# Kernel optimization log

Measured on AMD Instinct MI355X. Metric: run time of the kernel, lower is better.

The kernel has to match this reference:

```python
import jax, jax.numpy as jnp
import numpy as np

WSZ = 8          # window size (h == w)
DIM_HEAD = 32
EPS = 1e-5


def _rotate_half(t):
    t1, t2 = jnp.split(t, 2, axis=-1)
    return jnp.concatenate([-t2, t1], axis=-1)


def _window_rope(wsz_h, wsz_w, dim_head, base=10000.0):
    quarter = dim_head // 4
    freq = 1.0 / base ** (jnp.arange(quarter, dtype=jnp.float32) / quarter)
    th = jnp.arange(wsz_h, dtype=jnp.float32)[:, None] * freq[None, :]   # (wh, q)
    tw = jnp.arange(wsz_w, dtype=jnp.float32)[:, None] * freq[None, :]   # (ww, q)
    th = jnp.broadcast_to(th[:, None, :], (wsz_h, wsz_w, quarter)).reshape(wsz_h * wsz_w, quarter)
    tw = jnp.broadcast_to(tw[None, :, :], (wsz_h, wsz_w, quarter)).reshape(wsz_h * wsz_w, quarter)
    theta = jnp.concatenate([th, tw], axis=-1)                            # (L, d/2)
    cos = jnp.concatenate([jnp.cos(theta), jnp.cos(theta)], axis=-1)      # (L, d)
    sin = jnp.concatenate([jnp.sin(theta), jnp.sin(theta)], axis=-1)
    return cos, sin


def setup_inputs() -> dict:
    key = jax.random.key(0)
    k1, k2, k3 = jax.random.split(key, 3)
    B, D, H, W = 4, 512, 128, 128
    inner = 512  # heads * dim_head
    return {
        "x": jax.random.normal(k1, (B, D, H, W), dtype=jnp.float32),
        "ln_g": jnp.ones((D,), jnp.float32),
        "ln_b": jnp.zeros((D,), jnp.float32),
        "w_qkv": jax.random.normal(k2, (3 * inner, D), jnp.float32) * 0.02,
        "w_out": jax.random.normal(k3, (D, inner), jnp.float32) * 0.02,
        "b_out": jnp.zeros((D,), jnp.float32),
    }


def reference(x, ln_g, ln_b, w_qkv, w_out, b_out):
    B, D, H, W = x.shape
    wsz = WSZ
    dh = DIM_HEAD
    heads = D // dh
    nh, nw = H // wsz, W // wsz
    L = wsz * wsz
    shift = wsz // 2

    # channel LayerNorm (biased var over dim=1)
    mean = jnp.mean(x, axis=1, keepdims=True)
    var = jnp.var(x, axis=1, keepdims=True)
    xn = (x - mean) / jnp.sqrt(var + EPS) * ln_g[None, :, None, None] + ln_b[None, :, None, None]

    # shifted windows
    xs = jnp.roll(xn, shift=(-shift, -shift), axis=(-2, -1))
    # b d (h s1) (w s2) -> (b h w) d s1 s2
    xw = xs.reshape(B, D, nh, wsz, nw, wsz).transpose(0, 2, 4, 1, 3, 5)
    xw = xw.reshape(B * nh * nw, D, wsz, wsz)

    # 1x1 conv qkv (no bias)
    qkv = jnp.einsum('bdxy,ed->bexy', xw, w_qkv)           # (Bw, 3*inner, ws, ws)
    q, k, v = jnp.split(qkv, 3, axis=1)

    def to_heads(t):
        Bw = t.shape[0]
        return t.reshape(Bw, heads, dh, L).transpose(0, 1, 3, 2)  # (Bw, h, L, d)
    q, k, v = map(to_heads, (q, k, v))

    cos, sin = _window_rope(wsz, wsz, dh)
    cos = cos[None, None].astype(q.dtype)
    sin = sin[None, None].astype(q.dtype)
    q = q * cos + _rotate_half(q) * sin
    k = k * cos + _rotate_half(k) * sin

    scale = dh ** -0.5
    logits = jnp.einsum('bhid,bhjd->bhij', q, k) * scale
    attn = jax.nn.softmax(logits, axis=-1)
    out = jnp.einsum('bhij,bhjd->bhid', attn, v)            # (Bw, h, L, d)

    # b h (x y) d -> b (h d) x y
    out = out.transpose(0, 1, 3, 2).reshape(B * nh * nw, heads * dh, wsz, wsz)
    out = jnp.einsum('bdxy,ed->bexy', out, w_out) + b_out[None, :, None, None]

    # (b h w) d s1 s2 -> b d (h s1) (w s2)
    out = out.reshape(B, nh, nw, D, wsz, wsz).transpose(0, 3, 1, 4, 2, 5)
    out = out.reshape(B, D, H, W)
    out = jnp.roll(out, shift=(shift, shift), axis=(-2, -1))
    return out
```

## Files before the change

kernel.cpp:

```cpp
#include <hip/hip_runtime.h>
#include <hip/hip_bf16.h>

typedef unsigned short u16;
typedef __attribute__((ext_vector_type(8))) __bf16 bf16x8;
typedef __attribute__((ext_vector_type(4))) float f32x4;
typedef __attribute__((ext_vector_type(8))) unsigned short u16x8;

#define DEV __device__ __forceinline__

DEV float bf2f(u16 v){ union{unsigned u; float f;} c; c.u=((unsigned)v)<<16; return c.f; }
DEV u16 f2bf(float f){ union{float f; unsigned u;} c; c.f=f; unsigned r=c.u+0x7FFFu+((c.u>>16)&1u); return (u16)(r>>16); }
DEV f32x4 mfma16(bf16x8 a, bf16x8 b, f32x4 c){ return __builtin_amdgcn_mfma_f32_16x16x32_bf16(a,b,c,0,0,0); }


__global__ __launch_bounds__(256) void cvt_params_k(const float* __restrict__ wqkv, const float* __restrict__ wout,
                                                    const float* __restrict__ bout,
                                                    u16* __restrict__ wqkv_c, u16* __restrict__ wout_c,
                                                    u16* __restrict__ bout_c){
  int i = blockIdx.x*256 + threadIdx.x;
  if (i < 786432) wqkv_c[i] = f2bf(wqkv[i]);
  int j = i - 786432;
  if (j >= 0 && j < 262144) wout_c[j] = f2bf(wout[j]);
  int k = i - 1048576;
  if (k >= 0 && k < 512) bout_c[k] = f2bf(bout[k]);
}

__global__ __launch_bounds__(512) void ln_fused_k(const float* __restrict__ x, const float* __restrict__ g,
                                                  const float* __restrict__ bta, u16* __restrict__ A){
  __shared__ __align__(16) u16 tile[128*130];
  __shared__ float2 sstat[128];
  __shared__ float sg[512], sb2[512];
  float* reds = (float*)tile;
  float* redq = reds + 16*128;

  const int blk = blockIdx.x;
  const int b = blk >> 7, h_src = blk & 127;
  const int tid = threadIdx.x;
  const int wq = tid & 31, dr = tid >> 5;

  sg[tid]  = g[tid];
  sb2[tid] = bta[tid];

  const float* xp = x + ((size_t)(b*512)*128 + h_src)*128 + wq*4;

  float s0=0.f,s1=0.f,s2=0.f,s3=0.f, q0=0.f,q1=0.f,q2=0.f,q3=0.f;
  #pragma unroll 8
  for (int k = 0; k < 32; ++k){
    float4 v = *(const float4*)(xp + (size_t)(k*16 + dr)*16384);
    s0 += v.x; q0 += v.x*v.x;
    s1 += v.y; q1 += v.y*v.y;
    s2 += v.z; q2 += v.z*v.z;
    s3 += v.w; q3 += v.w*v.w;
  }
  *(float4*)&reds[dr*128 + wq*4] = make_float4(s0,s1,s2,s3);
  *(float4*)&redq[dr*128 + wq*4] = make_float4(q0,q1,q2,q3);
  __syncthreads();

  if (tid < 128){
    float s = 0.f, q = 0.f;
    #pragma unroll
    for (int r = 0; r < 16; ++r){ s += reds[r*128 + tid]; q += redq[r*128 + tid]; }
    float mean = s*(1.f/512.f);
    float rstd = rsqrtf(q*(1.f/512.f) - mean*mean + 1e-5f);
    sstat[tid] = make_float2(mean, rstd);
  }
  __syncthreads();

  const float2 st0 = sstat[wq*4+0];
  const float2 st1 = sstat[wq*4+1];
  const float2 st2 = sstat[wq*4+2];
  const float2 st3 = sstat[wq*4+3];

  const int h_out = (h_src - 4) & 127;
  const int mbase = ((b*16 + (h_out>>3))*16)*64 + (h_out&7)*8;
  const int seg = tid & 15, i0 = tid >> 4;

  for (int c = 0; c < 4; ++c){
    __syncthreads();
    #pragma unroll
    for (int k = 0; k < 8; ++k){
      const int d = c*128 + k*16 + dr;
      float4 v = *(const float4*)(xp + (size_t)d*16384);
      const float gg = sg[d], bb = sb2[d];
      u16* tr = tile + (size_t)(k*16 + dr)*130 + wq*4;
      tr[0] = f2bf((v.x - st0.x)*st0.y*gg + bb);
      tr[1] = f2bf((v.y - st1.x)*st1.y*gg + bb);
      tr[2] = f2bf((v.z - st2.x)*st2.y*gg + bb);
      tr[3] = f2bf((v.w - st3.x)*st3.y*gg + bb);
    }
    __syncthreads();
    #pragma unroll
    for (int p = 0; p < 4; ++p){
      const int i = p*32 + i0;
      const int w_out = (i - 4) & 127;
      const int m = mbase + (w_out>>3)*64 + (w_out&7);
      u16x8 o;
      #pragma unroll
      for (int jj = 0; jj < 8; ++jj) o[jj] = tile[(size_t)(seg*8 + jj)*130 + i];
      *(u16x8*)(A + (size_t)m*512 + c*128 + seg*8) = o;
    }
  }
}

template<bool BIAS>
__global__ __launch_bounds__(256) void gemm_nt_k(const u16* __restrict__ A, const u16* __restrict__ B,
                                                 const u16* __restrict__ bias, u16* __restrict__ C,
                                                 int M, int N, int K){
  __shared__ u16 As[128*32];
  __shared__ u16 Bs[128*32];
  const int tid = threadIdx.x, lane = tid & 63, wv = tid >> 6;
  const int q4 = lane >> 4, cc = lane & 15;
  const int m0 = blockIdx.y*128, n0 = blockIdx.x*128;
  const int wm = (wv >> 1)*64, wn = (wv & 1)*64;

  const int lrow = tid >> 2, lgrp = tid & 3;
  const u16* ag0 = A + (size_t)(m0 + lrow)*K + lgrp*8;
  const u16* ag1 = ag0 + (size_t)64*K;
  const u16* bg0 = B + (size_t)(n0 + lrow)*K + lgrp*8;
  const u16* bg1 = bg0 + (size_t)64*K;
  u16* as0 = As + tid*8;  u16* as1 = As + 2048 + tid*8;
  u16* bs0 = Bs + tid*8;  u16* bs1 = Bs + 2048 + tid*8;

  f32x4 acc[4][4] = {};
  for (int k0 = 0; k0 < K; k0 += 32){
    __builtin_amdgcn_global_load_lds(ag0 + k0, as0, 16, 0, 0);
    __builtin_amdgcn_global_load_lds(ag1 + k0, as1, 16, 0, 0);
    __builtin_amdgcn_global_load_lds(bg0 + k0, bs0, 16, 0, 0);
    __builtin_amdgcn_global_load_lds(bg1 + k0, bs1, 16, 0, 0);
    __syncthreads();
    bf16x8 af[4], bfr[4];
    #pragma unroll
    for (int t=0; t<4; ++t){
      u16x8 ta = *(const u16x8*)(As + (wm + t*16 + cc)*32 + q4*8);
      af[t]  = __builtin_bit_cast(bf16x8, ta);
      u16x8 tb = *(const u16x8*)(Bs + (wn + t*16 + cc)*32 + q4*8);
      bfr[t] = __builtin_bit_cast(bf16x8, tb);
    }
    #pragma unroll
    for (int i=0; i<4; ++i)
      #pragma unroll
      for (int j=0; j<4; ++j)
        acc[i][j] = mfma16(af[i], bfr[j], acc[i][j]);
    __syncthreads();
  }
  #pragma unroll
  for (int j=0; j<4; ++j){
    int col = n0 + wn + j*16 + cc;
    float bv = 0.f;
    if (BIAS) bv = bf2f(bias[col]);
    #pragma unroll
    for (int i=0; i<4; ++i){
      int rbase = m0 + wm + i*16 + q4*4;
      #pragma unroll
      for (int r=0; r<4; ++r)
        C[(size_t)(rbase + r)*N + col] = f2bf(acc[i][j][r] + bv);
    }
  }
}

__global__ __launch_bounds__(256) void attn_k(const u16* __restrict__ qkv, u16* __restrict__ O){
  __shared__ u16 Psh[4][64*72];
  const int tid = threadIdx.x, lane = tid & 63, wv = tid >> 6;
  const int q4 = lane >> 4, cc = lane & 15;
  const int w0 = blockIdx.x >> 2;
  const int hh = blockIdx.x & 3;
  const size_t base = (size_t)w0*64*1536;
  u16* Pw = Psh[wv];

  float freqj[8];
  #pragma unroll
  for (int j=0; j<8; ++j) freqj[j] = exp2f(-1.6609640474436811f * (float)j);
  const float sgn = (q4 < 2) ? -1.f : 1.f;
  const bool use_s2 = (q4 & 1) != 0;

  const int h = wv*4 + hh;
  bf16x8 qf[4], kf[4];
  #pragma unroll
  for (int t=0; t<4; ++t){
    const int l = t*16 + cc;
    const float sel = use_s2 ? (float)(l & 7) : (float)(l >> 3);
    u16x8 qr = *(const u16x8*)(qkv + base + (size_t)l*1536 + h*32 + q4*8);
    u16x8 kr = *(const u16x8*)(qkv + base + (size_t)l*1536 + 512 + h*32 + q4*8);
    u16x8 qo, ko;
    #pragma unroll
    for (int j=0; j<8; ++j){
      float qv = bf2f(qr[j]), kv = bf2f(kr[j]);
      float qp = __shfl_xor(qv, 32);
      float kp = __shfl_xor(kv, 32);
      float sn, cs; __sincosf(sel * freqj[j], &sn, &cs);
      qo[j] = f2bf(qv*cs + sgn*qp*sn);
      ko[j] = f2bf(kv*cs + sgn*kp*sn);
    }
    qf[t] = __builtin_bit_cast(bf16x8, qo);
    kf[t] = __builtin_bit_cast(bf16x8, ko);
  }
  f32x4 zero = {0.f, 0.f, 0.f, 0.f};
  f32x4 sacc[4][4];
  #pragma unroll
  for (int i=0; i<4; ++i)
    #pragma unroll
    for (int j=0; j<4; ++j)
      sacc[i][j] = mfma16(qf[i], kf[j], zero);
  const float scale = 0.17677669529663689f;
  #pragma unroll
  for (int i=0; i<4; ++i){
    #pragma unroll
    for (int r=0; r<4; ++r){
      float v0 = sacc[i][0][r]*scale, v1 = sacc[i][1][r]*scale;
      float v2 = sacc[i][2][r]*scale, v3 = sacc[i][3][r]*scale;
      float mx = fmaxf(fmaxf(v0,v1), fmaxf(v2,v3));
      #pragma unroll
      for (int msk=1; msk<16; msk<<=1) mx = fmaxf(mx, __shfl_xor(mx, msk));
      float e0 = __expf(v0-mx), e1 = __expf(v1-mx), e2 = __expf(v2-mx), e3 = __expf(v3-mx);
      float sm = e0+e1+e2+e3;
      #pragma unroll
      for (int msk=1; msk<16; msk<<=1) sm += __shfl_xor(sm, msk);
      float inv = 1.0f / sm;
      int row = i*16 + q4*4 + r;
      Pw[row*72 +      cc] = f2bf(e0*inv);
      Pw[row*72 + 16 + cc] = f2bf(e1*inv);
      Pw[row*72 + 32 + cc] = f2bf(e2*inv);
      Pw[row*72 + 48 + cc] = f2bf(e3*inv);
    }
  }
  f32x4 oacc[4][2] = {};
  #pragma unroll
  for (int s=0; s<2; ++s){
    bf16x8 vf[2];
    #pragma unroll
    for (int tn=0; tn<2; ++tn){
      u16x8 vv;
      #pragma unroll
      for (int j=0; j<8; ++j){
        int jr = s*32 + q4*8 + j;
        vv[j] = qkv[base + (size_t)jr*1536 + 1024 + h*32 + tn*16 + cc];
      }
      vf[tn] = __builtin_bit_cast(bf16x8, vv);
    }
    #pragma unroll
    for (int i=0; i<4; ++i){
      u16x8 pp = *(const u16x8*)(Pw + (i*16 + cc)*72 + s*32 + q4*8);
      bf16x8 pf = __builtin_bit_cast(bf16x8, pp);
      oacc[i][0] = mfma16(pf, vf[0], oacc[i][0]);
      oacc[i][1] = mfma16(pf, vf[1], oacc[i][1]);
    }
  }
  #pragma unroll
  for (int i=0; i<4; ++i)
    #pragma unroll
    for (int tn=0; tn<2; ++tn)
      #pragma unroll
      for (int r=0; r<4; ++r)
        O[(size_t)(w0*64 + i*16 + q4*4 + r)*512 + h*32 + tn*16 + cc] = f2bf(oacc[i][tn][r]);
}

__global__ __launch_bounds__(256) void unpermute_k(const u16* __restrict__ Cm, float* __restrict__ out){
  __shared__ u16 T[64*130];
  const int tid = threadIdx.x;
  const int hb = blockIdx.x;
  const int b  = blockIdx.y;
  const int ih = hb >> 3, s1 = hb & 7;
  const int h_out = (hb + 4) & 127;
  const int rid = tid >> 1, half = tid & 1;
  const int iw = rid >> 3, s2 = rid & 7;
  const size_t m = ((size_t)((b*16 + ih)*16 + iw))*64 + s1*8 + s2;
  const u16* src = Cm + m*512 + half*32;
  const int dl = tid >> 2, wseg = tid & 3;

  for (int c0=0; c0<512; c0+=64){
    #pragma unroll
    for (int v=0; v<4; ++v){
      u16x8 r = *(const u16x8*)(src + c0 + v*8);
      #pragma unroll
      for (int j=0; j<8; ++j) T[(half*32 + v*8 + j)*130 + rid] = r[j];
    }
    __syncthreads();
    float* dst = out + (((size_t)(b*512 + c0 + dl))*128 + h_out)*128 + wseg*32;
    #pragma unroll
    for (int v=0; v<4; ++v){
      f32x4 o0, o1;
      #pragma unroll
      for (int j=0; j<4; ++j){
        int w = wseg*32 + v*8 + j;
        o0[j] = bf2f(T[dl*130 + ((w - 4) & 127)]);
      }
      #pragma unroll
      for (int j=0; j<4; ++j){
        int w = wseg*32 + v*8 + 4 + j;
        o1[j] = bf2f(T[dl*130 + ((w - 4) & 127)]);
      }
      *(f32x4*)(dst + v*8)     = o0;
      *(f32x4*)(dst + v*8 + 4) = o1;
    }
    __syncthreads();
  }
}

extern "C" void kernel_launch(void* const* d_in, const int* in_sizes, int n_in,
                              void* d_out, int out_size, void* d_ws, size_t ws_size,
                              hipStream_t stream){
  (void)in_sizes; (void)n_in; (void)out_size; (void)ws_size;
  const float* x     = (const float*)d_in[0];
  const float* ln_g  = (const float*)d_in[1];
  const float* ln_b  = (const float*)d_in[2];
  const float* w_qkv = (const float*)d_in[3];
  const float* w_out = (const float*)d_in[4];
  const float* b_out = (const float*)d_in[5];
  char* ws = (char*)d_ws;

  u16* A      = (u16*)ws;
  u16* QKVc   = (u16*)(ws + 67108864);
  u16* wqkv_c = (u16*)(ws + 2*67108864);
  u16* wout_c = (u16*)(ws + 2*67108864 + 1572864);
  u16* bout_c = (u16*)(ws + 2*67108864 + 1572864 + 524288);

  cvt_params_k<<<4099, 256, 0, stream>>>(w_qkv, w_out, b_out, wqkv_c, wout_c, bout_c);
  ln_fused_k  <<<512, 512, 0, stream>>>(x, ln_g, ln_b, A);
  for (int c = 0; c < 4; ++c){
    u16* Ac = A + (size_t)c*16384*512;
    gemm_nt_k<false><<<dim3(12, 128), 256, 0, stream>>>(Ac, wqkv_c, (const u16*)nullptr, QKVc, 16384, 1536, 512);
    attn_k         <<<1024, 256, 0, stream>>>(QKVc, Ac);
  }
  gemm_nt_k<true> <<<dim3(4, 512), 256, 0, stream>>>(A, wout_c, bout_c, QKVc, 65536, 512, 512);
  unpermute_k <<<dim3(128, 4), 256, 0, stream>>>(QKVc, (float*)d_out);
}
```

Measured before the change: 634.6 us.

## Split LayerNorm statistics into a separate partial-sum kernel over channel groups

Moves the per-pixel mean/variance accumulation out of the fused LayerNorm kernel into a new kernel. That kernel reads x in contiguous spatial chunks per 32-channel group and writes partial sums and sums of squares to scratch, which the fused kernel then reduces over 16 groups. The aim is more coalesced, better-parallelised reads for the statistics pass than the strided per-row loop had. The cost is an extra launch and a partial-stats buffer written and read back, stored in the QKV scratch space. x is still read twice in total.

```diff
diff --git a/kernel.cpp b/kernel.cpp
--- a/kernel.cpp
+++ b/kernel.cpp
@@ -25,13 +25,41 @@
   if (k >= 0 && k < 512) bout_c[k] = f2bf(bout[k]);
 }
 
+__global__ __launch_bounds__(256) void ln_stats_k(const float* __restrict__ x, float* __restrict__ Pp){
+  const int blk = blockIdx.x;
+  const int q = blk & 3, bdg = blk >> 2;
+  const int b = bdg >> 4, dg = bdg & 15;
+  const int t = threadIdx.x;
+  const float* xp = x + ((size_t)b*512 + dg*32)*16384 + q*4096 + t*4;
+
+  f32x4 s0={0,0,0,0}, s1={0,0,0,0}, s2={0,0,0,0}, s3={0,0,0,0};
+  f32x4 q0={0,0,0,0}, q1={0,0,0,0}, q2={0,0,0,0}, q3={0,0,0,0};
+  #pragma unroll 4
+  for (int d = 0; d < 32; ++d){
+    const float* xd = xp + (size_t)d*16384;
+    f32x4 u0 = *(const f32x4*)(xd);
+    f32x4 u1 = *(const f32x4*)(xd + 1024);
+    f32x4 u2 = *(const f32x4*)(xd + 2048);
+    f32x4 u3 = *(const f32x4*)(xd + 3072);
+    s0 += u0; q0 += u0*u0;
+    s1 += u1; q1 += u1*u1;
+    s2 += u2; q2 += u2*u2;
+    s3 += u3; q3 += u3*u3;
+  }
+  float* Pb = Pp + (size_t)bdg*2*16384 + q*4096 + t*4;
+  *(f32x4*)(Pb       ) = s0;  *(f32x4*)(Pb + 1024) = s1;
+  *(f32x4*)(Pb + 2048) = s2;  *(f32x4*)(Pb + 3072) = s3;
+  *(f32x4*)(Pb + 16384       ) = q0;  *(f32x4*)(Pb + 16384 + 1024) = q1;
+  *(f32x4*)(Pb + 16384 + 2048) = q2;  *(f32x4*)(Pb + 16384 + 3072) = q3;
+}
+
 __global__ __launch_bounds__(512) void ln_fused_k(const float* __restrict__ x, const float* __restrict__ g,
-                                                  const float* __restrict__ bta, u16* __restrict__ A){
+                                                  const float* __restrict__ bta, u16* __restrict__ A,
+                                                  const float* __restrict__ Pp){
   __shared__ __align__(16) u16 tile[128*130];
+  __shared__ float red[2][128];
   __shared__ float2 sstat[128];
   __shared__ float sg[512], sb2[512];
-  float* reds = (float*)tile;
-  float* redq = reds + 16*128;
 
   const int blk = blockIdx.x;
   const int b = blk >> 7, h_src = blk & 127;
@@ -41,27 +69,18 @@
   sg[tid]  = g[tid];
   sb2[tid] = bta[tid];
 
-  const float* xp = x + ((size_t)(b*512)*128 + h_src)*128 + wq*4;
-
-  float s0=0.f,s1=0.f,s2=0.f,s3=0.f, q0=0.f,q1=0.f,q2=0.f,q3=0.f;
-  #pragma unroll 8
-  for (int k = 0; k < 32; ++k){
-    float4 v = *(const float4*)(xp + (size_t)(k*16 + dr)*16384);
-    s0 += v.x; q0 += v.x*v.x;
-    s1 += v.y; q1 += v.y*v.y;
-    s2 += v.z; q2 += v.z*v.z;
-    s3 += v.w; q3 += v.w*v.w;
-  }
-  *(float4*)&reds[dr*128 + wq*4] = make_float4(s0,s1,s2,s3);
-  *(float4*)&redq[dr*128 + wq*4] = make_float4(q0,q1,q2,q3);
+  if (tid < 256){
+    const int w = tid & 127, s = tid >> 7;
+    const float* pp = Pp + ((size_t)b*16*2 + s)*16384 + h_src*128 + w;
+    float acc = 0.f;
+    #pragma unroll
+    for (int dg = 0; dg < 16; ++dg) acc += pp[(size_t)dg*2*16384];
+    red[s][w] = acc;
+  }
   __syncthreads();
-
   if (tid < 128){
-    float s = 0.f, q = 0.f;
-    #pragma unroll
-    for (int r = 0; r < 16; ++r){ s += reds[r*128 + tid]; q += redq[r*128 + tid]; }
-    float mean = s*(1.f/512.f);
-    float rstd = rsqrtf(q*(1.f/512.f) - mean*mean + 1e-5f);
+    float mean = red[0][tid]*(1.f/512.f);
+    float rstd = rsqrtf(red[1][tid]*(1.f/512.f) - mean*mean + 1e-5f);
     sstat[tid] = make_float2(mean, rstd);
   }
   __syncthreads();
@@ -71,6 +90,7 @@
   const float2 st2 = sstat[wq*4+2];
   const float2 st3 = sstat[wq*4+3];
 
+  const float* xp = x + ((size_t)(b*512)*128 + h_src)*128 + wq*4;
   const int h_out = (h_src - 4) & 127;
   const int mbase = ((b*16 + (h_out>>3))*16)*64 + (h_out&7)*8;
   const int seg = tid & 15, i0 = tid >> 4;
@@ -313,9 +333,11 @@
   u16* wqkv_c = (u16*)(ws + 2*67108864);
   u16* wout_c = (u16*)(ws + 2*67108864 + 1572864);
   u16* bout_c = (u16*)(ws + 2*67108864 + 1572864 + 524288);
+  float* Pstats = (float*)QKVc;
 
   cvt_params_k<<<4099, 256, 0, stream>>>(w_qkv, w_out, b_out, wqkv_c, wout_c, bout_c);
-  ln_fused_k  <<<512, 512, 0, stream>>>(x, ln_g, ln_b, A);
+  ln_stats_k  <<<256, 256, 0, stream>>>(x, Pstats);
+  ln_fused_k  <<<512, 512, 0, stream>>>(x, ln_g, ln_b, A, Pstats);
   for (int c = 0; c < 4; ++c){
     u16* Ac = A + (size_t)c*16384*512;
     gemm_nt_k<false><<<dim3(12, 128), 256, 0, stream>>>(Ac, wqkv_c, (const u16*)nullptr, QKVc, 16384, 1536, 512);
```

After: 637.0 us. No clear change (+0.4%).
